# Optimization experiments

Hardware: AMD Instinct MI355X
Metric: run time of the kernel (lower is better)

## Reference

```python
import jax, jax.numpy as jnp
import numpy as np
from jax import lax

M1, M2 = 16, 16  # retained Fourier modes per spatial dim


def _spectral_conv(x, w1, w2):
    # x: [B, C, H, W] real; w1/w2: [C, C, M1, M2, 2] (re, im)
    B, C, H, W = x.shape
    xf = jnp.fft.rfft2(x, norm='ortho')            # [B, C, H, W//2+1] complex
    w1c = w1[..., 0] + 1j * w1[..., 1]
    w2c = w2[..., 0] + 1j * w2[..., 1]
    top = jnp.einsum('bixy,ioxy->boxy', xf[:, :, :M1, :M2], w1c)
    bot = jnp.einsum('bixy,ioxy->boxy', xf[:, :, -M1:, :M2], w2c)
    of = jnp.zeros((B, C, H, W // 2 + 1), dtype=xf.dtype)
    of = of.at[:, :, :M1, :M2].set(top).at[:, :, -M1:, :M2].set(bot)
    return jnp.fft.irfft2(of, s=(H, W), norm='ortho')


def _fno_block(x, w1, w2, skip_w):
    # spectral conv + linear (1x1 conv, no bias) skip
    return _spectral_conv(x, w1, w2) + jnp.einsum('bixy,io->boxy', x, skip_w)


def setup_inputs() -> dict:
    key = jax.random.key(0)
    ks = jax.random.split(key, 6)
    B, T, C, H, W = 4, 8, 64, 64, 64
    scale = 1.0 / (C * C)
    return {
        'x': jax.random.normal(ks[0], (B, T, C, H, W), dtype=jnp.float32),
        'sw1': jax.random.normal(ks[1], (6, C, C, M1, M2, 2), dtype=jnp.float32) * scale,
        'sw2': jax.random.normal(ks[2], (6, C, C, M1, M2, 2), dtype=jnp.float32) * scale,
        'skw': jax.random.normal(ks[3], (6, C, C), dtype=jnp.float32) * 0.02,
        'gate_b': jax.random.normal(ks[4], (3,), dtype=jnp.float32),
        'bias_h': jax.random.normal(ks[5], (1,), dtype=jnp.float32),
    }


def reference(x, sw1, sw2, skw, gate_b, bias_h):
    B, T, C, H, W = x.shape

    def f(i, inp):
        return _fno_block(inp, sw1[i], sw2[i], skw[i])

    def cell(xt, h):
        z = jax.nn.sigmoid(f(0, xt) + f(1, h) + gate_b[0])
        r = jax.nn.sigmoid(f(2, xt) + f(3, h) + gate_b[1])
        h_hat = jax.nn.selu(f(4, xt) + f(5, r * h) + gate_b[2])
        return (1.0 - z) * h + z * h_hat

    def step(h, xt):
        h = cell(xt, h)
        return h, None

    h0 = jnp.full((B, C, H, W), bias_h[0], dtype=x.dtype)
    h_final, _ = lax.scan(step, h0, jnp.moveaxis(x, 1, 0))  # scan over T
    return h_final  # return_sequences=False -> final hidden state [B, C, H, W]
```

## Files before the change

kernel.cpp:

```cpp
#include <hip/hip_runtime.h>

#define BB_ 4
#define TT_ 8
#define CC_ 64
#define HW 4096
#define UMAP 1024
#define STEP 0.09817477042468103f

#define OFF_UXALL 0
#define OFF_UH    (OFF_UXALL + TT_*256*UMAP)
#define OFF_URH   (OFF_UH + 256*UMAP)
#define OFF_SX    (OFF_URH + 256*UMAP)
#define OFF_SPART (OFF_SX + 3*TT_*256*UMAP)
#define OFF_H     (OFF_SPART + 2*8*256*UMAP)
#define OFF_Z     (OFF_H + BB_*CC_*HW)
#define OFF_RH    (OFF_Z + BB_*CC_*HW)
#define OFF_PH    (OFF_RH + BB_*CC_*HW)

__global__ __launch_bounds__(256) void k_init(float* __restrict__ hb,
                                              float* __restrict__ Uh,
                                              const float* __restrict__ bias_h) {
    float v = bias_h[0];
    int blk = blockIdx.x;
    if (blk < 1024) {
        int idx = (blk * 256 + threadIdx.x) * 4;
        *(float4*)(hb + idx) = make_float4(v, v, v, v);
    } else {
        int map = blk - 1024;
        float4 z = make_float4(0.f, 0.f, 0.f, 0.f);
        if (threadIdx.x == 0) z.x = 64.f * v;
        *(float4*)(Uh + (size_t)map * UMAP + threadIdx.x * 4) = z;
    }
}

__device__ __forceinline__ void dft_stages(const float* __restrict__ su,
                                           float* __restrict__ FxR, float* __restrict__ FxI,
                                           float* __restrict__ dst) {
    int tid = threadIdx.x;
    int kx = tid & 15, yb = tid >> 4;
    float stc, sts;
    __sincosf(-STEP * (float)kx, &sts, &stc);
    float wr = 1.f, wi = 0.f;
    float aR[4] = {0, 0, 0, 0}, aI[4] = {0, 0, 0, 0};
    for (int x = 0; x < 64; x++) {
        #pragma unroll
        for (int j = 0; j < 4; j++) {
            float v = su[(yb + 16 * j) * 65 + x];
            aR[j] = fmaf(v, wr, aR[j]);
            aI[j] = fmaf(v, wi, aI[j]);
        }
        float t = wr * stc - wi * sts;
        wi = wr * sts + wi * stc;
        wr = t;
    }
    #pragma unroll
    for (int j = 0; j < 4; j++) {
        FxR[(yb + 16 * j) * 16 + kx] = aR[j];
        FxI[(yb + 16 * j) * 16 + kx] = aI[j];
    }
    __syncthreads();
    int kb = tid >> 4;
    float c0, s0, c1, s1;
    __sincosf(-STEP * (float)kb, &s0, &c0);
    __sincosf(-STEP * (float)(kb + 48), &s1, &c1);
    float w0r = 1, w0i = 0, w1r = 1, w1i = 0;
    float A0r = 0, A0i = 0, A1r = 0, A1i = 0;
    for (int y = 0; y < 64; y++) {
        float Fr = FxR[y * 16 + kx], Fi = FxI[y * 16 + kx];
        A0r = fmaf(Fr, w0r, A0r); A0r = fmaf(-Fi, w0i, A0r);
        A0i = fmaf(Fr, w0i, A0i); A0i = fmaf(Fi, w0r, A0i);
        A1r = fmaf(Fr, w1r, A1r); A1r = fmaf(-Fi, w1i, A1r);
        A1i = fmaf(Fr, w1i, A1i); A1i = fmaf(Fi, w1r, A1i);
        float t0 = w0r * c0 - w0i * s0; w0i = w0r * s0 + w0i * c0; w0r = t0;
        float t1 = w1r * c1 - w1i * s1; w1i = w1r * s1 + w1i * c1; w1r = t1;
    }
    const float sc = 1.f / 64.f;
    float2* d2 = (float2*)dst;
    d2[kb * 16 + kx]        = make_float2(A0r * sc, A0i * sc);
    d2[(kb + 16) * 16 + kx] = make_float2(A1r * sc, A1i * sc);
}

__device__ __forceinline__ void dft_stages_512(const float* __restrict__ su,
                                               float* __restrict__ FxR, float* __restrict__ FxI,
                                               float* __restrict__ dst) {
    int tid = threadIdx.x;
    int kx = tid & 15, yb = tid >> 4;
    float stc, sts;
    __sincosf(-STEP * (float)kx, &sts, &stc);
    float wr = 1.f, wi = 0.f;
    float aR[2] = {0, 0}, aI[2] = {0, 0};
    for (int x = 0; x < 64; x++) {
        #pragma unroll
        for (int j = 0; j < 2; j++) {
            float v = su[(yb + 32 * j) * 65 + x];
            aR[j] = fmaf(v, wr, aR[j]);
            aI[j] = fmaf(v, wi, aI[j]);
        }
        float t = wr * stc - wi * sts;
        wi = wr * sts + wi * stc;
        wr = t;
    }
    #pragma unroll
    for (int j = 0; j < 2; j++) {
        FxR[(yb + 32 * j) * 16 + kx] = aR[j];
        FxI[(yb + 32 * j) * 16 + kx] = aI[j];
    }
    __syncthreads();
    int kb = tid >> 4;
    int ky = (kb < 16) ? kb : kb + 32;
    float c0, s0;
    __sincosf(-STEP * (float)ky, &s0, &c0);
    float w0r = 1, w0i = 0, A0r = 0, A0i = 0;
    for (int y = 0; y < 64; y++) {
        float Fr = FxR[y * 16 + kx], Fi = FxI[y * 16 + kx];
        A0r = fmaf(Fr, w0r, A0r); A0r = fmaf(-Fi, w0i, A0r);
        A0i = fmaf(Fr, w0i, A0i); A0i = fmaf(Fi, w0r, A0i);
        float t0 = w0r * c0 - w0i * s0; w0i = w0r * s0 + w0i * c0; w0r = t0;
    }
    const float sc = 1.f / 64.f;
    ((float2*)dst)[kb * 16 + kx] = make_float2(A0r * sc, A0i * sc);
}

__global__ __launch_bounds__(256) void k_dft_x(const float* __restrict__ x,
                                               float* __restrict__ Uxall) {
    __shared__ float su[64 * 65];
    __shared__ float FxR[1024], FxI[1024];
    int blk = blockIdx.x;
    int t = blk >> 8, map = blk & 255;
    int b = map >> 6, c = map & 63;
    const float* src = x + (((size_t)b * TT_ + t) * CC_ + c) * HW;
    int tid = threadIdx.x;
    #pragma unroll
    for (int k = 0; k < 4; k++) {
        int off = k * 1024 + tid * 4;
        float4 v = *(const float4*)(src + off);
        int y = off >> 6, xx = off & 63;
        su[y * 65 + xx + 0] = v.x; su[y * 65 + xx + 1] = v.y;
        su[y * 65 + xx + 2] = v.z; su[y * 65 + xx + 3] = v.w;
    }
    __syncthreads();
    dft_stages(su, FxR, FxI, Uxall + ((size_t)t * 256 + map) * UMAP);
}

__device__ __forceinline__ void mix_load(const float2* __restrict__ W2,
                                         const float2* __restrict__ U2, int i,
                                         float2 w[4], float2 u[4]) {
    const float2* wp = W2 + (size_t)i * 16384;
    const float2* up = U2 + (size_t)i * 512;
    w[0] = wp[0]; w[1] = wp[256]; w[2] = wp[512]; w[3] = wp[768];
    u[0] = up[0]; u[1] = up[32768]; u[2] = up[65536]; u[3] = up[98304];
}

__device__ __forceinline__ void mix_fma(const float2 w[4], const float2 u[4],
                                        float aR[4][4], float aI[4][4]) {
    #pragma unroll
    for (int oo = 0; oo < 4; oo++)
        #pragma unroll
        for (int bb = 0; bb < 4; bb++) {
            aR[oo][bb] = fmaf(u[bb].x, w[oo].x, aR[oo][bb]);
            aR[oo][bb] = fmaf(-u[bb].y, w[oo].y, aR[oo][bb]);
            aI[oo][bb] = fmaf(u[bb].x, w[oo].y, aI[oo][bb]);
            aI[oo][bb] = fmaf(u[bb].y, w[oo].x, aI[oo][bb]);
        }
}

__device__ __forceinline__ void mix_accum(const float2* __restrict__ W2,
                                          const float2* __restrict__ U2,
                                          int niter, float aR[4][4], float aI[4][4])
{
    float2 wA[4], uA[4], wB[4], uB[4], wN[4], uN[4];
    mix_load(W2, U2, 0, wA, uA);
    mix_load(W2, U2, 1, wB, uB);
    for (int i = 0; i + 2 < niter; i += 2) {
        mix_load(W2, U2, i + 2, wN, uN);
        mix_fma(wA, uA, aR, aI);
        #pragma unroll
        for (int k = 0; k < 4; k++) { wA[k] = wN[k]; uA[k] = uN[k]; }
        mix_load(W2, U2, i + 3, wN, uN);
        mix_fma(wB, uB, aR, aI);
        #pragma unroll
        for (int k = 0; k < 4; k++) { wB[k] = wN[k]; uB[k] = uN[k]; }
    }
    mix_fma(wA, uA, aR, aI);
    mix_fma(wB, uB, aR, aI);
}

__global__ __launch_bounds__(256, 4) void k_mix_x(
    const float* __restrict__ Uxall,
    const float* __restrict__ sw1, const float* __restrict__ sw2,
    float* __restrict__ Sx)
{
    __shared__ __align__(16) float2 Wl[2][640];
    int blk = blockIdx.x;
    int mq = blk & 15;
    int op = (blk >> 4) & 7;
    int half = (blk >> 7) & 1;
    int li = blk >> 8;
    int l = li * 2;
    int tid = threadIdx.x;
    int m0 = mq * 16;
    int o0 = op * 8;
    const float2* wsrc = (const float2*)(half ? sw2 : sw1);
    const float2* usrc = (const float2*)Uxall;

    int wl = tid & 7;
    int wrow = tid >> 3;
    int wii = wrow >> 3, woo = wrow & 7;
    const float4* wg4 = (const float4*)(wsrc
        + (((size_t)(l * 64 + wii) * 64) + o0 + woo) * 256 + m0) + wl;

    int mt = tid & 15, pp = tid >> 4;
    int tb0 = 2 * pp, tb1 = 2 * pp + 1;
    const float2* up0 = usrc + (size_t)(tb0 >> 2) * 131072
                        + (size_t)(tb0 & 3) * 32768 + half * 256 + m0 + mt;
    const float2* up1 = usrc + (size_t)(tb1 >> 2) * 131072
                        + (size_t)(tb1 & 3) * 32768 + half * 256 + m0 + mt;

    float aR[8][2], aI[8][2];
    #pragma unroll
    for (int oo = 0; oo < 8; oo++) {
        aR[oo][0] = 0.f; aR[oo][1] = 0.f;
        aI[oo][0] = 0.f; aI[oo][1] = 0.f;
    }

    float4 wv = wg4[0];
    Wl[0][(wii * 16 + 2 * wl) * 10 + woo]     = make_float2(wv.x, wv.y);
    Wl[0][(wii * 16 + 2 * wl + 1) * 10 + woo] = make_float2(wv.z, wv.w);
    wv = wg4[32768];
    __syncthreads();

    for (int c = 0; c < 16; ++c) {
        int cb = c & 1;
        float2 u0v[4], u1v[4];
        #pragma unroll
        for (int ii = 0; ii < 4; ii++) {
            u0v[ii] = up0[(size_t)(4 * c + ii) * 512];
            u1v[ii] = up1[(size_t)(4 * c + ii) * 512];
        }
        if (c < 15) {
            Wl[cb ^ 1][(wii * 16 + 2 * wl) * 10 + woo]     = make_float2(wv.x, wv.y);
            Wl[cb ^ 1][(wii * 16 + 2 * wl + 1) * 10 + woo] = make_float2(wv.z, wv.w);
            if (c < 14) wv = wg4[(size_t)(c + 2) * 32768];
        }
        #pragma unroll
        for (int ii = 0; ii < 4; ii++) {
            const float2* wrow2 = &Wl[cb][(ii * 16 + mt) * 10];
            float4 wq0 = *(const float4*)(wrow2 + 0);
            float4 wq1 = *(const float4*)(wrow2 + 2);
            float4 wq2 = *(const float4*)(wrow2 + 4);
            float4 wq3 = *(const float4*)(wrow2 + 6);
            float2 u0 = u0v[ii], u1 = u1v[ii];
            float2 wz[8];
            wz[0] = make_float2(wq0.x, wq0.y); wz[1] = make_float2(wq0.z, wq0.w);
            wz[2] = make_float2(wq1.x, wq1.y); wz[3] = make_float2(wq1.z, wq1.w);
            wz[4] = make_float2(wq2.x, wq2.y); wz[5] = make_float2(wq2.z, wq2.w);
            wz[6] = make_float2(wq3.x, wq3.y); wz[7] = make_float2(wq3.z, wq3.w);
            #pragma unroll
            for (int oo = 0; oo < 8; oo++) {
                float2 w = wz[oo];
                aR[oo][0] = fmaf(u0.x, w.x, aR[oo][0]);
                aR[oo][0] = fmaf(-u0.y, w.y, aR[oo][0]);
                aI[oo][0] = fmaf(u0.x, w.y, aI[oo][0]);
                aI[oo][0] = fmaf(u0.y, w.x, aI[oo][0]);
                aR[oo][1] = fmaf(u1.x, w.x, aR[oo][1]);
                aR[oo][1] = fmaf(-u1.y, w.y, aR[oo][1]);
                aI[oo][1] = fmaf(u1.x, w.y, aI[oo][1]);
                aI[oo][1] = fmaf(u1.y, w.x, aI[oo][1]);
            }
        }
        __syncthreads();
    }

    float2* S2 = (float2*)Sx;
    #pragma unroll
    for (int oo = 0; oo < 8; oo++)
        #pragma unroll
        for (int j = 0; j < 2; j++) {
            int tb = 2 * pp + j;
            int t = tb >> 2, b = tb & 3;
            S2[((size_t)(li * 8 + t) * 256 + b * 64 + o0 + oo) * 512
               + half * 256 + m0 + mt] = make_float2(aR[oo][j], aI[oo][j]);
        }
}

__device__ __forceinline__ void mix_body_h(int blk, int l0, int l1,
    const float* __restrict__ U,
    const float* __restrict__ sw1, const float* __restrict__ sw2,
    float* __restrict__ Spart)
{
    int og = blk & 15;
    int ic = (blk >> 4) & 7;
    int half = (blk >> 7) & 1;
    int g = (blk >> 8) & 1;
    int m = threadIdx.x;
    int o0 = og * 4, ib = ic * 8;
    int l = g ? l1 : l0;
    const float2* wt = (const float2*)(half ? sw2 : sw1);
    const float2* W2 = wt + (((size_t)l * 64 + ib) * 64 + o0) * 256 + m;
    const float2* U2 = (const float2*)U + (size_t)ib * 512 + half * 256 + m;
    float aR[4][4], aI[4][4];
    #pragma unroll
    for (int oo = 0; oo < 4; oo++)
        #pragma unroll
        for (int b = 0; b < 4; b++) { aR[oo][b] = 0.f; aI[oo][b] = 0.f; }
    mix_accum(W2, U2, 8, aR, aI);
    float2* S2 = (float2*)Spart;
    #pragma unroll
    for (int oo = 0; oo < 4; oo++)
        #pragma unroll
        for (int b = 0; b < 4; b++)
            S2[((size_t)(g * 8 + ic) * 256 + b * 64 + o0 + oo) * 512 + half * 256 + m]
                = make_float2(aR[oo][b], aI[oo][b]);
}

__device__ __forceinline__ void fma16(const float4 w, const float4 u, float acc[4][4]) {
    acc[0][0] = fmaf(u.x, w.x, acc[0][0]); acc[0][1] = fmaf(u.y, w.x, acc[0][1]);
    acc[0][2] = fmaf(u.z, w.x, acc[0][2]); acc[0][3] = fmaf(u.w, w.x, acc[0][3]);
    acc[1][0] = fmaf(u.x, w.y, acc[1][0]); acc[1][1] = fmaf(u.y, w.y, acc[1][1]);
    acc[1][2] = fmaf(u.z, w.y, acc[1][2]); acc[1][3] = fmaf(u.w, w.y, acc[1][3]);
    acc[2][0] = fmaf(u.x, w.z, acc[2][0]); acc[2][1] = fmaf(u.y, w.z, acc[2][1]);
    acc[2][2] = fmaf(u.z, w.z, acc[2][2]); acc[2][3] = fmaf(u.w, w.z, acc[2][3]);
    acc[3][0] = fmaf(u.x, w.w, acc[3][0]); acc[3][1] = fmaf(u.y, w.w, acc[3][1]);
    acc[3][2] = fmaf(u.z, w.w, acc[3][2]); acc[3][3] = fmaf(u.w, w.w, acc[3][3]);
}

__device__ __forceinline__ void skip_gemm(int rr, float* __restrict__ sW,
    const float* __restrict__ uA, long long bsA,
    const float* __restrict__ uB, long long bsB,
    const float* __restrict__ skw, int lA, int lB, float gb,
    float* __restrict__ out)
{
    int pxc = rr & 31, oh = (rr >> 5) & 1, b = rr >> 6;
    int tid = threadIdx.x;
    int ot = tid & 7, pt = tid >> 3;
    #pragma unroll
    for (int n = 0; n < 4; n++) {
        int idx = n * 1024 + tid * 4;
        int k = idx >> 5, oc = idx & 31;
        int p = k >> 6, i = k & 63;
        *(float4*)(sW + idx) =
            *(const float4*)(skw + (p ? lB : lA) * 4096 + i * 64 + oh * 32 + oc);
    }
    __syncthreads();
    float acc[4][4];
    #pragma unroll
    for (int oo = 0; oo < 4; oo++)
        #pragma unroll
        for (int q = 0; q < 4; q++) acc[oo][q] = 0.f;
    const float* pa = uA + (long long)b * bsA + pxc * 128 + pt * 4;
    const float* pb = uB + (long long)b * bsB + pxc * 128 + pt * 4;
    const float4* sW4 = (const float4*)sW;
    #pragma unroll 4
    for (int i = 0; i < 64; i++) {
        float4 ua = *(const float4*)(pa + (size_t)i * HW);
        float4 wa = sW4[i * 8 + ot];
        fma16(wa, ua, acc);
        float4 ub = *(const float4*)(pb + (size_t)i * HW);
        float4 wb = sW4[(64 + i) * 8 + ot];
        fma16(wb, ub, acc);
    }
    float* op = out + ((long long)(b * 64 + oh * 32 + ot * 4)) * HW + pxc * 128 + pt * 4;
    #pragma unroll
    for (int oo = 0; oo < 4; oo++) {
        float4 r = make_float4(acc[oo][0] + gb, acc[oo][1] + gb,
                               acc[oo][2] + gb, acc[oo][3] + gb);
        *(float4*)(op + (size_t)oo * HW) = r;
    }
}

__device__ __forceinline__ void idft_stage1_256(const float* __restrict__ SR,
                                                const float* __restrict__ SI,
                                                float* __restrict__ GR, float* __restrict__ GI)
{
    int tid = threadIdx.x;
    int kx = tid & 15, yb = tid >> 4;
    #pragma unroll
    for (int j = 0; j < 4; j++) {
        int y = yb + 16 * j;
        float stc, sts;
        __sincosf(STEP * (float)y, &sts, &stc);
        float ar = 0.f, ai = 0.f;
        float wr = 1.f, wi = 0.f;
        for (int k = 0; k < 16; k++) {
            float sr_ = SR[k * 16 + kx], si_ = SI[k * 16 + kx];
            ar = fmaf(sr_, wr, ar); ar = fmaf(-si_, wi, ar);
            ai = fmaf(sr_, wi, ai); ai = fmaf(si_, wr, ai);
            float t = wr * stc - wi * sts; wi = wr * sts + wi * stc; wr = t;
        }
        int q = (3 * y) & 3;
        float w2r = (q == 0) ? 1.f : ((q == 2) ? -1.f : 0.f);
        float w2i = (q == 1) ? 1.f : ((q == 3) ? -1.f : 0.f);
        for (int k = 16; k < 32; k++) {
            float sr_ = SR[k * 16 + kx], si_ = SI[k * 16 + kx];
            ar = fmaf(sr_, w2r, ar); ar = fmaf(-si_, w2i, ar);
            ai = fmaf(sr_, w2i, ai); ai = fmaf(si_, w2r, ai);
            float t = w2r * stc - w2i * sts; w2i = w2r * sts + w2i * stc; w2r = t;
        }
        GR[y * 16 + kx] = ar;
        GI[y * 16 + kx] = ai;
    }
}

__device__ __forceinline__ void z_finalize(int map, int t,
    const float* __restrict__ Spart, const float* __restrict__ Sx,
    float* __restrict__ zb, float* __restrict__ smem)
{
    float* SR = smem;
    float* SI = smem + 512;
    float* GR = smem + 1024;
    float* GI = smem + 2048;
    int tid = threadIdx.x;
    {
        float4 v = ((const float4*)Sx)[((size_t)t * 256 + map) * 256 + tid];
        float sxr = v.x, sxi = v.y, syr = v.z, syi = v.w;
        const float4* base = (const float4*)Spart;
        #pragma unroll
        for (int ic = 0; ic < 8; ic++) {
            float4 p = base[((size_t)ic * 256 + map) * 256 + tid];
            sxr += p.x; sxi += p.y; syr += p.z; syi += p.w;
        }
        SR[2 * tid] = sxr; SI[2 * tid] = sxi;
        SR[2 * tid + 1] = syr; SI[2 * tid + 1] = syi;
    }
    __syncthreads();
    idft_stage1_256(SR, SI, GR, GI);
    __syncthreads();
    int x = tid & 63, ybase = tid >> 6;
    float cx, sx;
    __sincosf(STEP * (float)x, &sx, &cx);
    size_t mo = (size_t)map * HW;
    #pragma unroll
    for (int j = 0; j < 16; j++) {
        int y = ybase + 4 * j;
        float acc = GR[y * 16];
        float wr = cx, wi = sx;
        #pragma unroll
        for (int k = 1; k < 16; k++) {
            acc = fmaf(2.f * GR[y * 16 + k], wr, acc);
            acc = fmaf(-2.f * GI[y * 16 + k], wi, acc);
            float t2 = wr * cx - wi * sx; wi = wr * sx + wi * cx; wr = t2;
        }
        float val = acc * (1.f / 64.f);
        int idx = y * 64 + x;
        float pre = val + zb[mo + idx];
        zb[mo + idx] = 1.f / (1.f + __expf(-pre));
    }
}

__global__ __launch_bounds__(256) void k_front_zr(
    const float* __restrict__ Uh,
    const float* __restrict__ xt, const float* __restrict__ hb,
    const float* __restrict__ sw1, const float* __restrict__ sw2,
    const float* __restrict__ skw, const float* __restrict__ gate_b,
    float* __restrict__ Spart, float* __restrict__ zb, float* __restrict__ rhb)
{
    __shared__ float smem[4096];
    int blk = blockIdx.x;
    if (blk < 512) {
        mix_body_h(blk, 1, 3, Uh, sw1, sw2, Spart);
    } else {
        int r = blk - 512;
        int g = r >> 8;
        skip_gemm(r & 255, smem,
                  xt, (long long)TT_ * CC_ * HW, hb, (long long)CC_ * HW,
                  skw, g ? 2 : 0, g ? 3 : 1, gate_b[g], g ? rhb : zb);
    }
}

__global__ __launch_bounds__(256) void k_front_h(
    const float* __restrict__ Urh,
    const float* __restrict__ xt, const float* __restrict__ rhb,
    const float* __restrict__ sw1, const float* __restrict__ sw2,
    const float* __restrict__ skw, const float* __restrict__ gate_b,
    float* __restrict__ Spart, float* __restrict__ phb,
    const float* __restrict__ Sx, int t, float* __restrict__ zb)
{
    __shared__ float smem[4096];
    int blk = blockIdx.x;
    if (blk < 256) {
        z_finalize(blk, t, Spart, Sx, zb, smem);
    } else if (blk < 512) {
        mix_body_h(blk, 5, 5, Urh, sw1, sw2, Spart);
    } else {
        int r = blk - 512;
        skip_gemm(r, smem,
                  xt, (long long)TT_ * CC_ * HW, rhb, (long long)CC_ * HW,
                  skw, 4, 5, gate_b[2], phb);
    }
}

__device__ __forceinline__ void idft_stage1_512(const float* __restrict__ SR,
                                                const float* __restrict__ SI,
                                                float* __restrict__ GR, float* __restrict__ GI)
{
    int tid = threadIdx.x;
    int kx = tid & 15, yb = tid >> 4;
    #pragma unroll
    for (int j = 0; j < 2; j++) {
        int y = yb + 32 * j;
        float stc, sts;
        __sincosf(STEP * (float)y, &sts, &stc);
        float ar = 0.f, ai = 0.f;
        float wr = 1.f, wi = 0.f;
        for (int k = 0; k < 16; k++) {
            float sr_ = SR[k * 16 + kx], si_ = SI[k * 16 + kx];
            ar = fmaf(sr_, wr, ar); ar = fmaf(-si_, wi, ar);
            ai = fmaf(sr_, wi, ai); ai = fmaf(si_, wr, ai);
            float t = wr * stc - wi * sts; wi = wr * sts + wi * stc; wr = t;
        }
        int q = (3 * y) & 3;
        float w2r = (q == 0) ? 1.f : ((q == 2) ? -1.f : 0.f);
        float w2i = (q == 1) ? 1.f : ((q == 3) ? -1.f : 0.f);
        for (int k = 16; k < 32; k++) {
            float sr_ = SR[k * 16 + kx], si_ = SI[k * 16 + kx];
            ar = fmaf(sr_, w2r, ar); ar = fmaf(-si_, w2i, ar);
            ai = fmaf(sr_, w2i, ai); ai = fmaf(si_, w2r, ai);
            float t = w2r * stc - w2i * sts; w2i = w2r * sts + w2i * stc; w2r = t;
        }
        GR[y * 16 + kx] = ar;
        GI[y * 16 + kx] = ai;
    }
}

__global__ __launch_bounds__(512) void k_back_zr(
    const float* __restrict__ Spart, const float* __restrict__ Sx, int t,
    float* __restrict__ rhb,
    const float* __restrict__ hb, float* __restrict__ Urh)
{
    __shared__ float smem[6208];
    float* SR = smem;
    float* SI = smem + 512;
    float* GR = smem + 1024;
    float* GI = smem + 2048;
    int map = blockIdx.x;
    int tid = threadIdx.x;
    {
        float2 v = ((const float2*)Sx)[((size_t)(8 + t) * 256 + map) * 512 + tid];
        float sr = v.x, si = v.y;
        const float2* base = (const float2*)Spart;
        #pragma unroll
        for (int ic = 0; ic < 8; ic++) {
            float2 p = base[((size_t)(8 + ic) * 256 + map) * 512 + tid];
            sr += p.x; si += p.y;
        }
        SR[tid] = sr; SI[tid] = si;
    }
    __syncthreads();
    idft_stage1_512(SR, SI, GR, GI);
    __syncthreads();
    int x = tid & 63, ybase = tid >> 6;
    float cx, sx;
    __sincosf(STEP * (float)x, &sx, &cx);
    size_t mo = (size_t)map * HW;
    float rhv[8];
    #pragma unroll
    for (int j = 0; j < 8; j++) {
        int y = ybase + 8 * j;
        float acc = GR[y * 16];
        float wr = cx, wi = sx;
        #pragma unroll
        for (int k = 1; k < 16; k++) {
            acc = fmaf(2.f * GR[y * 16 + k], wr, acc);
            acc = fmaf(-2.f * GI[y * 16 + k], wi, acc);
            float t2 = wr * cx - wi * sx; wi = wr * sx + wi * cx; wr = t2;
        }
        float val = acc * (1.f / 64.f);
        int idx = y * 64 + x;
        float pre = val + rhb[mo + idx];
        float rr = 1.f / (1.f + __expf(-pre));
        float rh = rr * hb[mo + idx];
        rhb[mo + idx] = rh;
        rhv[j] = rh;
    }
    __syncthreads();
    float* su = smem;
    #pragma unroll
    for (int j = 0; j < 8; j++) {
        int y = ybase + 8 * j;
        su[y * 65 + x] = rhv[j];
    }
    __syncthreads();
    dft_stages_512(su, smem + 4160, smem + 5184, Urh + (size_t)map * UMAP);
}

__global__ __launch_bounds__(512) void k_back_h(
    const float* __restrict__ Spart, const float* __restrict__ Sx, int t,
    const float* __restrict__ zb, const float* __restrict__ phb,
    float* __restrict__ hb, float* __restrict__ Uh)
{
    __shared__ float smem[6208];
    float* SR = smem;
    float* SI = smem + 512;
    float* GR = smem + 1024;
    float* GI = smem + 2048;
    int map = blockIdx.x & 255;
    int tid = threadIdx.x;
    {
        float2 v = ((const float2*)Sx)[((size_t)(2 * 8 + t) * 256 + map) * 512 + tid];
        float sr = v.x, si = v.y;
        const float2* base = (const float2*)Spart;
        #pragma unroll
        for (int ic = 0; ic < 8; ic++) {
            float2 p = base[((size_t)(8 + ic) * 256 + map) * 512 + tid];
            sr += p.x; si += p.y;
        }
        SR[tid] = sr; SI[tid] = si;
    }
    __syncthreads();
    idft_stage1_512(SR, SI, GR, GI);
    __syncthreads();
    int x = tid & 63, ybase = tid >> 6;
    float cx, sx;
    __sincosf(STEP * (float)x, &sx, &cx);
    size_t mo = (size_t)map * HW;
    float hv[8];
    #pragma unroll
    for (int j = 0; j < 8; j++) {
        int y = ybase + 8 * j;
        float acc = GR[y * 16];
        float wr = cx, wi = sx;
        #pragma unroll
        for (int k = 1; k < 16; k++) {
            acc = fmaf(2.f * GR[y * 16 + k], wr, acc);
            acc = fmaf(-2.f * GI[y * 16 + k], wi, acc);
            float t2 = wr * cx - wi * sx; wi = wr * sx + wi * cx; wr = t2;
        }
        float val = acc * (1.f / 64.f);
        int idx = y * 64 + x;
        float pre = val + phb[mo + idx];
        float hh = (pre > 0.f) ? 1.0507009873554805f * pre
                               : 1.7580993408473766f * (__expf(pre) - 1.f);
        float z = zb[mo + idx];
        float hn = fmaf(z, hh - hb[mo + idx], hb[mo + idx]);
        hb[mo + idx] = hn;
        hv[j] = hn;
    }
    __syncthreads();
    float* su = smem;
    #pragma unroll
    for (int j = 0; j < 8; j++) {
        int y = ybase + 8 * j;
        su[y * 65 + x] = hv[j];
    }
    __syncthreads();
    dft_stages_512(su, smem + 4160, smem + 5184, Uh + (size_t)map * UMAP);
}

extern "C" void kernel_launch(void* const* d_in, const int* in_sizes, int n_in,
                              void* d_out, int out_size, void* d_ws, size_t ws_size,
                              hipStream_t stream)
{
    (void)in_sizes; (void)n_in; (void)out_size; (void)ws_size;
    const float* x   = (const float*)d_in[0];
    const float* sw1 = (const float*)d_in[1];
    const float* sw2 = (const float*)d_in[2];
    const float* skw = (const float*)d_in[3];
    const float* gb  = (const float*)d_in[4];
    const float* bh  = (const float*)d_in[5];
    float* ws    = (float*)d_ws;
    float* Uxall = ws + OFF_UXALL;
    float* Uh    = ws + OFF_UH;
    float* Urh   = ws + OFF_URH;
    float* Sx    = ws + OFF_SX;
    float* Sp    = ws + OFF_SPART;
    float* hb    = ws + OFF_H;
    float* zb    = ws + OFF_Z;
    float* rhb   = ws + OFF_RH;
    float* phb   = ws + OFF_PH;

    k_init<<<1280, 256, 0, stream>>>(hb, Uh, bh);
    k_dft_x<<<2048, 256, 0, stream>>>(x, Uxall);
    k_mix_x<<<768, 256, 0, stream>>>(Uxall, sw1, sw2, Sx);
    for (int t = 0; t < TT_; t++) {
        const float* xt = x + (size_t)t * CC_ * HW;
        k_front_zr<<<1024, 256, 0, stream>>>(Uh, xt, hb, sw1, sw2, skw, gb,
                                             Sp, zb, rhb);
        k_back_zr<<<256, 512, 0, stream>>>(Sp, Sx, t, rhb, hb, Urh);
        k_front_h<<<768, 256, 0, stream>>>(Urh, xt, rhb, sw1, sw2, skw, gb,
                                           Sp, phb, Sx, t, zb);
        k_back_h<<<256, 512, 0, stream>>>(Sp, Sx, t, zb, phb, hb, Uh);
    }
    hipMemcpyAsync(d_out, hb, (size_t)BB_ * CC_ * HW * sizeof(float),
                   hipMemcpyDeviceToDevice, stream);
}
```

Measured before the change: 741.9 us.

## Stage U tiles in LDS for x-mix and cut h-mix input-channel split to 2

New measurement: 739.3 us. No clear change (-0.3%).

```diff
diff --git a/kernel.cpp b/kernel.cpp
--- a/kernel.cpp
+++ b/kernel.cpp
@@ -190,7 +190,8 @@
     const float* __restrict__ sw1, const float* __restrict__ sw2,
     float* __restrict__ Sx)
 {
-    __shared__ __align__(16) float2 Wl[2][640];
+    __shared__ float4 Wt4[2][256];
+    __shared__ float4 Ut4[2][1024];
     int blk = blockIdx.x;
     int mq = blk & 15;
     int op = (blk >> 4) & 7;
@@ -208,14 +209,11 @@
     int wii = wrow >> 3, woo = wrow & 7;
     const float4* wg4 = (const float4*)(wsrc
         + (((size_t)(l * 64 + wii) * 64) + o0 + woo) * 256 + m0) + wl;
+    int ut_ = wrow >> 2, ub_ = wrow & 3;
+    const float4* ug4 = (const float4*)(usrc
+        + (size_t)ut_ * 131072 + (size_t)ub_ * 32768 + half * 256 + m0) + wl;
 
     int mt = tid & 15, pp = tid >> 4;
-    int tb0 = 2 * pp, tb1 = 2 * pp + 1;
-    const float2* up0 = usrc + (size_t)(tb0 >> 2) * 131072
-                        + (size_t)(tb0 & 3) * 32768 + half * 256 + m0 + mt;
-    const float2* up1 = usrc + (size_t)(tb1 >> 2) * 131072
-                        + (size_t)(tb1 & 3) * 32768 + half * 256 + m0 + mt;
-
     float aR[8][2], aI[8][2];
     #pragma unroll
     for (int oo = 0; oo < 8; oo++) {
@@ -223,41 +221,37 @@
         aI[oo][0] = 0.f; aI[oo][1] = 0.f;
     }
 
-    float4 wv = wg4[0];
-    Wl[0][(wii * 16 + 2 * wl) * 10 + woo]     = make_float2(wv.x, wv.y);
-    Wl[0][(wii * 16 + 2 * wl + 1) * 10 + woo] = make_float2(wv.z, wv.w);
-    wv = wg4[32768];
-    __syncthreads();
+    float4 wv  = wg4[0];
+    float4 uv0 = ug4[0];
+    float4 uv1 = ug4[256];
+    float4 uv2 = ug4[512];
+    float4 uv3 = ug4[768];
 
     for (int c = 0; c < 16; ++c) {
         int cb = c & 1;
-        float2 u0v[4], u1v[4];
+        Wt4[cb][tid] = wv;
+        Ut4[cb][tid] = uv0;
+        Ut4[cb][256 + tid] = uv1;
+        Ut4[cb][512 + tid] = uv2;
+        Ut4[cb][768 + tid] = uv3;
+        if (c < 15) {
+            size_t ib = (size_t)(c + 1) * 4;
+            wv  = wg4[ib * 8192];
+            uv0 = ug4[ib * 256];
+            uv1 = ug4[(ib + 1) * 256];
+            uv2 = ug4[(ib + 2) * 256];
+            uv3 = ug4[(ib + 3) * 256];
+        }
+        __syncthreads();
+        const float2* Wl = (const float2*)Wt4[cb];
+        const float2* Ul = (const float2*)Ut4[cb];
         #pragma unroll
         for (int ii = 0; ii < 4; ii++) {
-            u0v[ii] = up0[(size_t)(4 * c + ii) * 512];
-            u1v[ii] = up1[(size_t)(4 * c + ii) * 512];
-        }
-        if (c < 15) {
-            Wl[cb ^ 1][(wii * 16 + 2 * wl) * 10 + woo]     = make_float2(wv.x, wv.y);
-            Wl[cb ^ 1][(wii * 16 + 2 * wl + 1) * 10 + woo] = make_float2(wv.z, wv.w);
-            if (c < 14) wv = wg4[(size_t)(c + 2) * 32768];
-        }
-        #pragma unroll
-        for (int ii = 0; ii < 4; ii++) {
-            const float2* wrow2 = &Wl[cb][(ii * 16 + mt) * 10];
-            float4 wq0 = *(const float4*)(wrow2 + 0);
-            float4 wq1 = *(const float4*)(wrow2 + 2);
-            float4 wq2 = *(const float4*)(wrow2 + 4);
-            float4 wq3 = *(const float4*)(wrow2 + 6);
-            float2 u0 = u0v[ii], u1 = u1v[ii];
-            float2 wz[8];
-            wz[0] = make_float2(wq0.x, wq0.y); wz[1] = make_float2(wq0.z, wq0.w);
-            wz[2] = make_float2(wq1.x, wq1.y); wz[3] = make_float2(wq1.z, wq1.w);
-            wz[4] = make_float2(wq2.x, wq2.y); wz[5] = make_float2(wq2.z, wq2.w);
-            wz[6] = make_float2(wq3.x, wq3.y); wz[7] = make_float2(wq3.z, wq3.w);
+            float2 u0 = Ul[(ii * 32 + 2 * pp) * 16 + mt];
+            float2 u1 = Ul[(ii * 32 + 2 * pp + 1) * 16 + mt];
             #pragma unroll
             for (int oo = 0; oo < 8; oo++) {
-                float2 w = wz[oo];
+                float2 w = Wl[(ii * 8 + oo) * 16 + mt];
                 aR[oo][0] = fmaf(u0.x, w.x, aR[oo][0]);
                 aR[oo][0] = fmaf(-u0.y, w.y, aR[oo][0]);
                 aI[oo][0] = fmaf(u0.x, w.y, aI[oo][0]);
@@ -283,18 +277,16 @@
         }
 }
 
-__device__ __forceinline__ void mix_body_h(int blk, int l0, int l1,
+__device__ __forceinline__ void mix_body2(int r, int l, int slotbase,
     const float* __restrict__ U,
     const float* __restrict__ sw1, const float* __restrict__ sw2,
     float* __restrict__ Spart)
 {
-    int og = blk & 15;
-    int ic = (blk >> 4) & 7;
-    int half = (blk >> 7) & 1;
-    int g = (blk >> 8) & 1;
+    int og = r & 15;
+    int ic = (r >> 4) & 1;
+    int half = r >> 5;
     int m = threadIdx.x;
-    int o0 = og * 4, ib = ic * 8;
-    int l = g ? l1 : l0;
+    int o0 = og * 4, ib = ic * 32;
     const float2* wt = (const float2*)(half ? sw2 : sw1);
     const float2* W2 = wt + (((size_t)l * 64 + ib) * 64 + o0) * 256 + m;
     const float2* U2 = (const float2*)U + (size_t)ib * 512 + half * 256 + m;
@@ -303,13 +295,14 @@
     for (int oo = 0; oo < 4; oo++)
         #pragma unroll
         for (int b = 0; b < 4; b++) { aR[oo][b] = 0.f; aI[oo][b] = 0.f; }
-    mix_accum(W2, U2, 8, aR, aI);
+    mix_accum(W2, U2, 32, aR, aI);
+    int slot = slotbase + ic;
     float2* S2 = (float2*)Spart;
     #pragma unroll
     for (int oo = 0; oo < 4; oo++)
         #pragma unroll
         for (int b = 0; b < 4; b++)
-            S2[((size_t)(g * 8 + ic) * 256 + b * 64 + o0 + oo) * 512 + half * 256 + m]
+            S2[((size_t)slot * 256 + b * 64 + o0 + oo) * 512 + half * 256 + m]
                 = make_float2(aR[oo][b], aI[oo][b]);
 }
 
@@ -415,7 +408,7 @@
         float sxr = v.x, sxi = v.y, syr = v.z, syi = v.w;
         const float4* base = (const float4*)Spart;
         #pragma unroll
-        for (int ic = 0; ic < 8; ic++) {
+        for (int ic = 0; ic < 2; ic++) {
             float4 p = base[((size_t)ic * 256 + map) * 256 + tid];
             sxr += p.x; sxi += p.y; syr += p.z; syi += p.w;
         }
@@ -456,10 +449,11 @@
 {
     __shared__ float smem[4096];
     int blk = blockIdx.x;
-    if (blk < 512) {
-        mix_body_h(blk, 1, 3, Uh, sw1, sw2, Spart);
+    if (blk < 128) {
+        int g = blk >> 6;
+        mix_body2(blk & 63, g ? 3 : 1, g * 2, Uh, sw1, sw2, Spart);
     } else {
-        int r = blk - 512;
+        int r = blk - 128;
         int g = r >> 8;
         skip_gemm(r & 255, smem,
                   xt, (long long)TT_ * CC_ * HW, hb, (long long)CC_ * HW,
@@ -477,12 +471,12 @@
 {
     __shared__ float smem[4096];
     int blk = blockIdx.x;
-    if (blk < 256) {
-        z_finalize(blk, t, Spart, Sx, zb, smem);
-    } else if (blk < 512) {
-        mix_body_h(blk, 5, 5, Urh, sw1, sw2, Spart);
+    if (blk < 64) {
+        mix_body2(blk, 5, 4, Urh, sw1, sw2, Spart);
+    } else if (blk < 320) {
+        z_finalize(blk - 64, t, Spart, Sx, zb, smem);
     } else {
-        int r = blk - 512;
+        int r = blk - 320;
         skip_gemm(r, smem,
                   xt, (long long)TT_ * CC_ * HW, rhb, (long long)CC_ * HW,
                   skw, 4, 5, gate_b[2], phb);
@@ -539,8 +533,8 @@
         float sr = v.x, si = v.y;
         const float2* base = (const float2*)Spart;
         #pragma unroll
-        for (int ic = 0; ic < 8; ic++) {
-            float2 p = base[((size_t)(8 + ic) * 256 + map) * 512 + tid];
+        for (int s = 2; s < 4; s++) {
+            float2 p = base[((size_t)s * 256 + map) * 512 + tid];
             sr += p.x; si += p.y;
         }
         SR[tid] = sr; SI[tid] = si;
@@ -600,8 +594,8 @@
         float sr = v.x, si = v.y;
         const float2* base = (const float2*)Spart;
         #pragma unroll
-        for (int ic = 0; ic < 8; ic++) {
-            float2 p = base[((size_t)(8 + ic) * 256 + map) * 512 + tid];
+        for (int s = 4; s < 6; s++) {
+            float2 p = base[((size_t)s * 256 + map) * 512 + tid];
             sr += p.x; si += p.y;
         }
         SR[tid] = sr; SI[tid] = si;
@@ -673,10 +667,10 @@
     k_mix_x<<<768, 256, 0, stream>>>(Uxall, sw1, sw2, Sx);
     for (int t = 0; t < TT_; t++) {
         const float* xt = x + (size_t)t * CC_ * HW;
-        k_front_zr<<<1024, 256, 0, stream>>>(Uh, xt, hb, sw1, sw2, skw, gb,
-                                             Sp, zb, rhb);
+        k_front_zr<<<640, 256, 0, stream>>>(Uh, xt, hb, sw1, sw2, skw, gb,
+                                            Sp, zb, rhb);
         k_back_zr<<<256, 512, 0, stream>>>(Sp, Sx, t, rhb, hb, Urh);
-        k_front_h<<<768, 256, 0, stream>>>(Urh, xt, rhb, sw1, sw2, skw, gb,
+        k_front_h<<<576, 256, 0, stream>>>(Urh, xt, rhb, sw1, sw2, skw, gb,
                                            Sp, phb, Sx, t, zb);
         k_back_h<<<256, 512, 0, stream>>>(Sp, Sx, t, zb, phb, hb, Uh);
     }
```
